# Kernel optimization log

Hardware: AMD Instinct MI355X
Metric: run time of the kernel (lower is better)

## Reference

```python
import jax, jax.numpy as jnp
import numpy as np

N, E, CIN, H = 100000, 1600000, 128, 128


def setup_inputs() -> dict:
    key = jax.random.key(0)
    ks = jax.random.split(key, 10)
    return {
        "x": jax.random.normal(ks[0], (N, CIN), dtype=jnp.float32),
        "edge_index": jax.random.randint(ks[1], (2, E), 0, N, dtype=jnp.int64),
        "edge_weight": jax.random.uniform(ks[2], (E,), dtype=jnp.float32),
        "h_prev": jax.random.normal(ks[3], (N, H), dtype=jnp.float32),
        "c_prev": jax.random.normal(ks[4], (N, H), dtype=jnp.float32),
        "Wx0": jax.random.normal(ks[5], (4, CIN, H), dtype=jnp.float32) * 0.05,
        "Wx1": jax.random.normal(ks[6], (4, CIN, H), dtype=jnp.float32) * 0.05,
        "Wh0": jax.random.normal(ks[7], (4, H, H), dtype=jnp.float32) * 0.05,
        "Wh1": jax.random.normal(ks[8], (4, H, H), dtype=jnp.float32) * 0.05,
        "bx": jnp.zeros((4, H), dtype=jnp.float32),
        "bh": jnp.zeros((4, H), dtype=jnp.float32),
    }


def _scaled_laplacian_norm(edge_index, edge_weight, n):
    # PyG ChebConv norm with lambda_max=2.0, sym normalization:
    # L_hat = 2L/lambda_max - I = -D^{-1/2} A D^{-1/2} (zero diagonal).
    src, dst = edge_index[0], edge_index[1]
    deg = jax.ops.segment_sum(edge_weight, src, num_segments=n)
    safe = jnp.where(deg > 0, deg, 1.0)
    dis = jnp.where(deg > 0, 1.0 / jnp.sqrt(safe), 0.0)  # deg_inv_sqrt, inf->0
    norm = -(dis[src] * edge_weight * dis[dst])
    return src, dst, norm


def _propagate(feat, src, dst, norm, n):
    # (L_hat @ feat)[i] = sum_{e: dst_e=i} norm_e * feat[src_e]
    return jax.ops.segment_sum(feat[src] * norm[:, None], dst, num_segments=n)


def reference(x, edge_index, edge_weight, h_prev, c_prev, Wx0, Wx1, Wh0, Wh1, bx, bh):
    n = x.shape[0]
    src, dst, norm = _scaled_laplacian_norm(edge_index, edge_weight, n)
    # Shared Chebyshev propagation across all 4 gates (K=2: T0=I, T1=L_hat)
    Lx = _propagate(x, src, dst, norm, n)          # [N, CIN]
    Lh = _propagate(h_prev, src, dst, norm, n)     # [N, H]
    gates = (
        jnp.einsum("nc,gch->gnh", x, Wx0)
        + jnp.einsum("nc,gch->gnh", Lx, Wx1)
        + jnp.einsum("nd,gdh->gnh", h_prev, Wh0)
        + jnp.einsum("nd,gdh->gnh", Lh, Wh1)
        + bx[:, None, :] + bh[:, None, :]
    )  # [4, N, H]
    i = jax.nn.sigmoid(gates[0])
    f = jax.nn.sigmoid(gates[1])
    g = jnp.tanh(gates[2])
    o = jax.nn.sigmoid(gates[3])
    c_t = f * c_prev + i * g
    h_t = o * jnp.tanh(c_t)
    return (h_t, c_t)
```

## Files before the change

kernel.cpp:

```cpp
#include <hip/hip_runtime.h>
#include <hip/hip_bf16.h>

#define NN   100000
#define NE   1600000
#define MPAD 100096
#define BK   64

typedef __attribute__((ext_vector_type(8))) short bf16x8;
typedef __attribute__((ext_vector_type(4))) float f32x4;
typedef __attribute__((ext_vector_type(8))) unsigned short u16x8;

#define OFF_DEG  0ull
#define OFF_CUR  400384ull
#define OFF_XH   800768ull
#define OFF_FP   52049920ull
#define OFF_WT   103299072ull
#define OFF_BIAS 103823360ull

__device__ __forceinline__ unsigned short f2bf(float f) {
    unsigned int u = __float_as_uint(f);
    u += 0x7fffu + ((u >> 16) & 1u);
    return (unsigned short)(u >> 16);
}
__device__ __forceinline__ float bf2f(unsigned short u) {
    return __uint_as_float(((unsigned int)u) << 16);
}
__device__ __forceinline__ float sigf(float x)  { return 1.f / (1.f + __expf(-x)); }
__device__ __forceinline__ float tanhf_(float x){ return 1.f - 2.f / (__expf(2.f * x) + 1.f); }

typedef __attribute__((address_space(3))) void lds_void;
typedef __attribute__((address_space(1))) void g_void;
__device__ __forceinline__ void gload16(const void* g, void* l) {
    __builtin_amdgcn_global_load_lds((const g_void*)g, (lds_void*)l, 16, 0, 0);
}

__global__ void zero_packw_kernel(float4* __restrict__ z,
                                  const float* __restrict__ Wx0, const float* __restrict__ Wx1,
                                  const float* __restrict__ Wh0, const float* __restrict__ Wh1,
                                  const float* __restrict__ bx,  const float* __restrict__ bh,
                                  unsigned short* __restrict__ Wt, float* __restrict__ bias) {
    int b = blockIdx.x;
    if (b < 196) {
        int t = b * 256 + threadIdx.x;
        if (t < 50048) z[t] = make_float4(0.f, 0.f, 0.f, 0.f);
        return;
    }
    int t = (b - 196) * 256 + threadIdx.x;
    int col = t >> 9, k = t & 511;
    int h = col >> 2, g = col & 3;
    const float* W; int kk;
    if      (k < 128) { W = Wx0; kk = k; }
    else if (k < 256) { W = Wx1; kk = k - 128; }
    else if (k < 384) { W = Wh0; kk = k - 256; }
    else              { W = Wh1; kk = k - 384; }
    float v = W[((size_t)(g << 7) + kk) * 128 + h];
    Wt[(size_t)col * 512 + k] = f2bf(v);
    if (k == 0) bias[col] = bx[(g << 7) + h] + bh[(g << 7) + h];
}

#define EB 1563
#define CVT_BLOCKS 25024
__global__ void mega1_kernel(const int* __restrict__ src, const int* __restrict__ dst,
                             const float* __restrict__ ew,
                             float* __restrict__ deg, int* __restrict__ cursor,
                             uint2* __restrict__ bkt,
                             const float* __restrict__ x, const float* __restrict__ hp,
                             unsigned short* __restrict__ XH) {
    int b = blockIdx.x;
    if (b < EB) {
        int e0 = b * 1024 + threadIdx.x;
        int sarr[4], darr[4]; float warr[4]; bool ok[4];
#pragma unroll
        for (int k = 0; k < 4; ++k) {
            int e = e0 + k * 256;
            ok[k] = (e < NE);
            if (ok[k]) { sarr[k] = src[e]; darr[k] = dst[e]; warr[k] = ew[e]; }
        }
#pragma unroll
        for (int k = 0; k < 4; ++k)
            if (ok[k]) atomicAdd(&deg[sarr[k]], warr[k]);
        int pos[4];
#pragma unroll
        for (int k = 0; k < 4; ++k)
            if (ok[k]) pos[k] = atomicAdd(&cursor[darr[k]], 1);
#pragma unroll
        for (int k = 0; k < 4; ++k)
            if (ok[k] && pos[k] < BK) {
                uint2 v; v.x = (unsigned)sarr[k]; v.y = __float_as_uint(warr[k]);
                bkt[((size_t)darr[k] << 6) + pos[k]] = v;
            }
        return;
    }
    int t = (b - EB) * 256 + threadIdx.x;
    int n = t >> 6, q = t & 63;
    ushort4 o = make_ushort4(0, 0, 0, 0);
    if (n < NN) {
        const float* s = (q < 32) ? (x + (size_t)n * 128 + (q << 2))
                                  : (hp + (size_t)n * 128 + ((q - 32) << 2));
        float4 v = *(const float4*)s;
        o = make_ushort4(f2bf(v.x), f2bf(v.y), f2bf(v.z), f2bf(v.w));
    }
    *(ushort4*)(XH + (size_t)n * 256 + (q << 2)) = o;
}

__launch_bounds__(256)
__global__ void gather_pack_kernel(const float* __restrict__ deg,
                                   const int* __restrict__ cursor,
                                   const uint2* __restrict__ bkt,
                                   const unsigned short* __restrict__ XH,
                                   unsigned short* __restrict__ Fp) {
    int node = (blockIdx.x * 256 + threadIdx.x) >> 6;
    int lane = threadIdx.x & 63;
    if (node >= MPAD) return;
    const int g  = lane >> 3;
    const int li = lane & 7;
    unsigned short* Frow = Fp + (size_t)node * 256;
    if (node >= NN) {
        if (g < 4) *(uint4*)(Frow + li * 32 + g * 8) = make_uint4(0, 0, 0, 0);
        return;
    }
    int cnt = cursor[node];
    cnt = cnt > BK ? BK : cnt;
    float dd = deg[node];
    float disd = dd > 0.f ? rsqrtf(dd) : 0.f;
    const uint2* row = bkt + ((size_t)node << 6);
    float acc[32];
#pragma unroll
    for (int k = 0; k < 32; ++k) acc[k] = 0.f;

    int e = g;
    uint2 ce;
    if (e < cnt) ce = row[e];
    while (e < cnt) {
        uint2 cur = ce;
        int en = e + 8;
        if (en < cnt) ce = row[en];
        float dsv = deg[cur.x];
        const unsigned short* xr = XH + (size_t)cur.x * 256 + li * 32;
        u16x8 v0 = *(const u16x8*)(xr);
        u16x8 v1 = *(const u16x8*)(xr + 8);
        u16x8 v2 = *(const u16x8*)(xr + 16);
        u16x8 v3 = *(const u16x8*)(xr + 24);
        float diss = dsv > 0.f ? rsqrtf(dsv) : 0.f;
        float nm = -(diss * __uint_as_float(cur.y) * disd);
#pragma unroll
        for (int k = 0; k < 8; ++k) acc[k]      += nm * bf2f((unsigned short)v0[k]);
#pragma unroll
        for (int k = 0; k < 8; ++k) acc[k + 8]  += nm * bf2f((unsigned short)v1[k]);
#pragma unroll
        for (int k = 0; k < 8; ++k) acc[k + 16] += nm * bf2f((unsigned short)v2[k]);
#pragma unroll
        for (int k = 0; k < 8; ++k) acc[k + 24] += nm * bf2f((unsigned short)v3[k]);
        e = en;
    }
#pragma unroll
    for (int k = 0; k < 32; ++k) {
        acc[k] += __shfl_xor(acc[k], 8, 64);
        acc[k] += __shfl_xor(acc[k], 16, 64);
        acc[k] += __shfl_xor(acc[k], 32, 64);
    }
    if (g < 4) {
        u16x8 o;
#pragma unroll
        for (int k = 0; k < 8; ++k)
            o[k] = f2bf(acc[g * 8 + k]);
        *(u16x8*)(Frow + li * 32 + g * 8) = o;
    }
}

__device__ __forceinline__ f32x4 shflx4(f32x4 v, int m) {
    f32x4 r;
    r[0] = __shfl_xor(v[0], m, 64);
    r[1] = __shfl_xor(v[1], m, 64);
    r[2] = __shfl_xor(v[2], m, 64);
    r[3] = __shfl_xor(v[3], m, 64);
    return r;
}
__device__ __forceinline__ float sel4(f32x4 v, int k) {
    float r = v[0];
    r = (k == 1) ? v[1] : r;
    r = (k == 2) ? v[2] : r;
    r = (k == 3) ? v[3] : r;
    return r;
}
__device__ __forceinline__ float pick4(float a0, float a1, float a2, float a3, int k) {
    float r = a0;
    r = (k == 1) ? a1 : r;
    r = (k == 2) ? a2 : r;
    r = (k == 3) ? a3 : r;
    return r;
}

#define WAITV(n)  asm volatile("s_waitcnt vmcnt(" #n ")" ::: "memory")
#define WAITLGKM0 asm volatile("s_waitcnt lgkmcnt(0)" ::: "memory")

__launch_bounds__(256)
__global__ void gemm_lstm_kernel(const unsigned short* __restrict__ XHu,
                                 const unsigned short* __restrict__ Fpu,
                                 const unsigned short* __restrict__ Wtu,
                                 const float* __restrict__ bias,
                                 const float* __restrict__ c_prev,
                                 float* __restrict__ out) {
    __shared__ __align__(16) short sa[4 * 4096];
    __shared__ __align__(16) short sb[4 * 4096];

    const int tid  = threadIdx.x;
    const int lane = tid & 63;
    const int wave = tid >> 6;
    const int wm = wave >> 1, wn = wave & 1;
    const int lr = lane & 15, lq = lane >> 4;

    const int b = blockIdx.x;
    const int ntile = (b >> 3) & 3;
    const int mtile = (b & 7) | ((b >> 5) << 3);
    if (mtile >= 782) return;
    const size_t m0 = (size_t)mtile * 128;
    const int n0 = ntile * 128;

    const short* XH = (const short*)XHu;
    const short* Fp = (const short*)Fpu;
    const short* Wt = (const short*)Wtu;

    const int arow = tid >> 2;
    const int sx   = (((tid & 3) ^ ((arow >> 1) & 3)) << 3);
    const size_t rowA = (m0 + arow) * 256 + sx;
    const short* gB = Wt + (size_t)(n0 + arow) * 512 + sx;

    const int rbase = wm * 64 + lq * 4 + (lr & 3);
    const int hbase = (n0 >> 2) + wn * 16 + (lr >> 2);

    const int xr = (lr >> 1) & 3;
    int offA[4], offB[4];
#pragma unroll
    for (int i = 0; i < 4; ++i) {
        offA[i] = (wm * 64 + i * 16 + lr) * 32 + ((lq ^ xr) << 3);
        offB[i] = (wn * 64 + i * 16 + lr) * 32 + ((lq ^ xr) << 3);
    }

    f32x4 acc[4][4];
#pragma unroll
    for (int i = 0; i < 4; ++i)
#pragma unroll
        for (int j = 0; j < 4; ++j) acc[i][j] = (f32x4){0.f, 0.f, 0.f, 0.f};

    auto stage = [&](int kt) {
        const int buf = (kt & 3) << 12;
        const int off = ((kt >> 3) << 7) + ((kt & 3) << 5);
        const short* Ab = ((kt >> 2) & 1) ? Fp : XH;
        gload16(Ab + rowA + off,            &sa[buf + wave * 512]);
        gload16(Ab + rowA + 64 * 256 + off, &sa[buf + 2048 + wave * 512]);
        gload16(gB + kt * 32,               &sb[buf + wave * 512]);
        gload16(gB + kt * 32 + 64 * 512,    &sb[buf + 2048 + wave * 512]);
    };

    stage(0); stage(1); stage(2);

#pragma unroll
    for (int kt = 0; kt < 16; ++kt) {
        if      (kt <= 13) WAITV(8);
        else if (kt == 14) WAITV(4);
        else               WAITV(0);
        __builtin_amdgcn_sched_barrier(0);
        __builtin_amdgcn_s_barrier();
        if (kt + 3 < 16) stage(kt + 3);
        const int buf = (kt & 3) << 12;
        bf16x8 af[4], bfr[4];
#pragma unroll
        for (int i = 0; i < 4; ++i) af[i]  = *(const bf16x8*)&sa[buf + offA[i]];
#pragma unroll
        for (int i = 0; i < 4; ++i) bfr[i] = *(const bf16x8*)&sb[buf + offB[i]];
        __builtin_amdgcn_s_setprio(1);
#pragma unroll
        for (int i = 0; i < 4; ++i)
#pragma unroll
            for (int j = 0; j < 4; ++j)
                acc[i][j] = __builtin_amdgcn_mfma_f32_16x16x32_bf16(af[i], bfr[j], acc[i][j], 0, 0, 0);
        __builtin_amdgcn_s_setprio(0);
        WAITLGKM0;
        __builtin_amdgcn_sched_barrier(0);
    }

    float bs[4];
#pragma unroll
    for (int j = 0; j < 4; ++j) bs[j] = bias[n0 + wn * 64 + j * 16 + lr];
    float cp[4][4];
#pragma unroll
    for (int i = 0; i < 4; ++i) {
        size_t grow = m0 + rbase + i * 16;
#pragma unroll
        for (int j = 0; j < 4; ++j)
            cp[i][j] = (grow < NN) ? c_prev[grow * 128 + hbase + j * 4] : 0.f;
    }

    const int k = lr & 3;
#pragma unroll
    for (int i = 0; i < 4; ++i) {
        size_t grow = m0 + rbase + i * 16;
        if (grow >= NN) continue;
#pragma unroll
        for (int j = 0; j < 4; ++j) {
            f32x4 v0 = acc[i][j];
            v0[0] += bs[j]; v0[1] += bs[j]; v0[2] += bs[j]; v0[3] += bs[j];
            f32x4 v1 = shflx4(v0, 1);
            f32x4 v2 = shflx4(v0, 2);
            f32x4 v3 = shflx4(v0, 3);
            float vv0 = sel4(v0, k), vv1 = sel4(v1, k),
                  vv2 = sel4(v2, k), vv3 = sel4(v3, k);
            float gi = pick4(vv0, vv1, vv2, vv3, k);
            float gf = pick4(vv0, vv1, vv2, vv3, k ^ 1);
            float gg = pick4(vv0, vv1, vv2, vv3, k ^ 2);
            float go = pick4(vv0, vv1, vv2, vv3, k ^ 3);
            float iv = sigf(gi), fv = sigf(gf), gv = tanhf_(gg), ov = sigf(go);
            float ct = fv * cp[i][j] + iv * gv;
            float ht = ov * tanhf_(ct);
            int h = hbase + j * 4;
            out[grow * 128 + h] = ht;
            out[(size_t)NN * 128 + grow * 128 + h] = ct;
        }
    }
}

extern "C" void kernel_launch(void* const* d_in, const int* in_sizes, int n_in,
                              void* d_out, int out_size, void* d_ws, size_t ws_size,
                              hipStream_t stream) {
    const float* x      = (const float*)d_in[0];
    const int*   ei     = (const int*)  d_in[1];
    const float* ew     = (const float*)d_in[2];
    const float* h_prev = (const float*)d_in[3];
    const float* c_prev = (const float*)d_in[4];
    const float* Wx0    = (const float*)d_in[5];
    const float* Wx1    = (const float*)d_in[6];
    const float* Wh0    = (const float*)d_in[7];
    const float* Wh1    = (const float*)d_in[8];
    const float* bx     = (const float*)d_in[9];
    const float* bh     = (const float*)d_in[10];
    float* out = (float*)d_out;

    char* ws = (char*)d_ws;
    float*          deg    = (float*)(ws + OFF_DEG);
    int*            cursor = (int*)  (ws + OFF_CUR);
    unsigned short* XH     = (unsigned short*)(ws + OFF_XH);
    unsigned short* Fp     = (unsigned short*)(ws + OFF_FP);
    unsigned short* Wt     = (unsigned short*)(ws + OFF_WT);
    float*          bias   = (float*)(ws + OFF_BIAS);
    uint2*          bkt    = (uint2*)d_out;

    const int* src = ei;
    const int* dst = ei + NE;

    zero_packw_kernel<<<196 + 1024, 256, 0, stream>>>(
        (float4*)ws, Wx0, Wx1, Wh0, Wh1, bx, bh, Wt, bias);

    mega1_kernel<<<EB + CVT_BLOCKS, 256, 0, stream>>>(
        src, dst, ew, deg, cursor, bkt, x, h_prev, XH);

    gather_pack_kernel<<<MPAD / 4, 256, 0, stream>>>(deg, cursor, bkt, XH, Fp);

    gemm_lstm_kernel<<<3136, 256, 0, stream>>>(XH, Fp, Wt, bias, c_prev, out);
}
```

Before: 628.0 us.

## Restructure gather kernel: wave-wide edge load, shuffle broadcast, 16-lane row split

The gather-pack kernel now loads all 64 bucket entries and their source degrees at once, one per lane, and computes the normalization per lane. Each edge's source id and norm are then broadcast with shuffles, replacing a serial per-edge load chain. Rows are split across 16 lanes of 16 bf16 each, so 4 edges are processed per step, and each lane keeps four edges' loads in flight before accumulating. This is meant to raise memory-level parallelism and cut the reduction shuffles and accumulator registers, at the cost of extra shuffles and some idle lanes when a node has few edges.

```diff
diff --git a/kernel.cpp b/kernel.cpp
--- a/kernel.cpp
+++ b/kernel.cpp
@@ -112,59 +112,64 @@
     int node = (blockIdx.x * 256 + threadIdx.x) >> 6;
     int lane = threadIdx.x & 63;
     if (node >= MPAD) return;
-    const int g  = lane >> 3;
-    const int li = lane & 7;
+    const int g  = lane >> 4;
+    const int li = lane & 15;
     unsigned short* Frow = Fp + (size_t)node * 256;
     if (node >= NN) {
-        if (g < 4) *(uint4*)(Frow + li * 32 + g * 8) = make_uint4(0, 0, 0, 0);
+        if (g < 2) *(uint4*)(Frow + li * 16 + g * 8) = make_uint4(0, 0, 0, 0);
         return;
     }
     int cnt = cursor[node];
     cnt = cnt > BK ? BK : cnt;
     float dd = deg[node];
     float disd = dd > 0.f ? rsqrtf(dd) : 0.f;
-    const uint2* row = bkt + ((size_t)node << 6);
-    float acc[32];
-#pragma unroll
-    for (int k = 0; k < 32; ++k) acc[k] = 0.f;
-
-    int e = g;
-    uint2 ce;
-    if (e < cnt) ce = row[e];
-    while (e < cnt) {
-        uint2 cur = ce;
-        int en = e + 8;
-        if (en < cnt) ce = row[en];
-        float dsv = deg[cur.x];
-        const unsigned short* xr = XH + (size_t)cur.x * 256 + li * 32;
-        u16x8 v0 = *(const u16x8*)(xr);
-        u16x8 v1 = *(const u16x8*)(xr + 8);
-        u16x8 v2 = *(const u16x8*)(xr + 16);
-        u16x8 v3 = *(const u16x8*)(xr + 24);
-        float diss = dsv > 0.f ? rsqrtf(dsv) : 0.f;
-        float nm = -(diss * __uint_as_float(cur.y) * disd);
-#pragma unroll
-        for (int k = 0; k < 8; ++k) acc[k]      += nm * bf2f((unsigned short)v0[k]);
-#pragma unroll
-        for (int k = 0; k < 8; ++k) acc[k + 8]  += nm * bf2f((unsigned short)v1[k]);
-#pragma unroll
-        for (int k = 0; k < 8; ++k) acc[k + 16] += nm * bf2f((unsigned short)v2[k]);
-#pragma unroll
-        for (int k = 0; k < 8; ++k) acc[k + 24] += nm * bf2f((unsigned short)v3[k]);
-        e = en;
-    }
-#pragma unroll
-    for (int k = 0; k < 32; ++k) {
-        acc[k] += __shfl_xor(acc[k], 8, 64);
+
+    uint2 ent = bkt[((size_t)node << 6) + lane];
+    int   sid_l = (lane < cnt) ? (int)ent.x : 0;
+    float w_l   = __uint_as_float(ent.y);
+    float dsv   = deg[sid_l];
+    float dis_s = dsv > 0.f ? rsqrtf(dsv) : 0.f;
+    float nrm_l = (lane < cnt) ? -(dis_s * w_l * disd) : 0.f;
+
+    float acc[16];
+#pragma unroll
+    for (int k = 0; k < 16; ++k) acc[k] = 0.f;
+
+    for (int base = 0; base < cnt; base += 16) {
+        u16x8 va[4][2]; float nm[4]; bool on[4];
+#pragma unroll
+        for (int r = 0; r < 4; ++r) {
+            int e = base + r * 4 + g;
+            on[r] = (e < cnt);
+            int   sid = __shfl(sid_l, e & 63, 64);
+            float nr  = __shfl(nrm_l, e & 63, 64);
+            nm[r] = nr;
+            if (on[r]) {
+                const unsigned short* xr = XH + (size_t)sid * 256 + li * 16;
+                va[r][0] = *(const u16x8*)(xr);
+                va[r][1] = *(const u16x8*)(xr + 8);
+            }
+        }
+#pragma unroll
+        for (int r = 0; r < 4; ++r) {
+            if (!on[r]) continue;
+#pragma unroll
+            for (int k = 0; k < 8; ++k) acc[k]     += nm[r] * bf2f((unsigned short)va[r][0][k]);
+#pragma unroll
+            for (int k = 0; k < 8; ++k) acc[k + 8] += nm[r] * bf2f((unsigned short)va[r][1][k]);
+        }
+    }
+#pragma unroll
+    for (int k = 0; k < 16; ++k) {
         acc[k] += __shfl_xor(acc[k], 16, 64);
         acc[k] += __shfl_xor(acc[k], 32, 64);
     }
-    if (g < 4) {
+    if (g < 2) {
         u16x8 o;
 #pragma unroll
         for (int k = 0; k < 8; ++k)
-            o[k] = f2bf(acc[g * 8 + k]);
-        *(u16x8*)(Frow + li * 32 + g * 8) = o;
+            o[k] = f2bf((g & 1) ? acc[k + 8] : acc[k]);
+        *(u16x8*)(Frow + li * 16 + g * 8) = o;
     }
 }
 
```

New measurement: 650.0 us. +3.5%, slower.
